# Kernel optimization log

Hardware: AMD Instinct MI355X
Metric: run time of the kernel (lower is better)

Reference implementation:

```python
import jax, jax.numpy as jnp
import numpy as np

N_NODES = 50000


def _gcn_layer(x, W, b, src, dst, n_nodes):
    # x: [N, Fin] -> h: [N, Fout]
    h = x @ W
    # symmetric normalization deg^{-1/2} A_hat deg^{-1/2} (self-loops already in src/dst)
    deg = jax.ops.segment_sum(jnp.ones(src.shape[0], h.dtype), dst, num_segments=n_nodes)
    dis = jnp.where(deg > 0, jax.lax.rsqrt(deg), jnp.zeros_like(deg))
    norm = dis[src] * dis[dst]  # [E]
    msg = h[src] * norm[:, None]  # [E, Fout]
    out = jax.ops.segment_sum(msg, dst, num_segments=n_nodes)
    return out + b


def setup_inputs() -> dict:
    key = jax.random.key(0)
    k1, k2, k3, k4 = jax.random.split(key, 4)
    in_ch, hid, out_ch = 128, 128, 64
    x = jax.random.normal(k1, (N_NODES, in_ch), dtype=jnp.float32)
    edge_index = jax.random.randint(k2, (2, 800000), 0, N_NODES, dtype=jnp.int64)
    # glorot-style init for the linear weights
    W1 = jax.random.normal(k3, (in_ch, hid), dtype=jnp.float32) * (1.0 / np.sqrt(in_ch))
    b1 = jnp.zeros((hid,), dtype=jnp.float32)
    W2 = jax.random.normal(k4, (hid, out_ch), dtype=jnp.float32) * (1.0 / np.sqrt(hid))
    b2 = jnp.zeros((out_ch,), dtype=jnp.float32)
    return {"x": x, "edge_index": edge_index, "W1": W1, "b1": b1, "W2": W2, "b2": b2}


def reference(x, edge_index, W1, b1, W2, b2):
    n = x.shape[0]
    loops = jnp.arange(n, dtype=edge_index.dtype)
    src = jnp.concatenate([edge_index[0], loops])
    dst = jnp.concatenate([edge_index[1], loops])
    h = jnp.tanh(_gcn_layer(x, W1, b1, src, dst, n))
    return _gcn_layer(h, W2, b2, src, dst, n)
```

## Files before the change

### kernel.cpp

```cpp
#include <hip/hip_runtime.h>
#include <hip/hip_fp16.h>
#include <math.h>


__global__ __launch_bounds__(256) void normalize_kernel(const int* __restrict__ ei32,
                                                        int* __restrict__ out, int n2,
                                                        int* __restrict__ hist, int nh) {
    __shared__ int s_is64;
    if (threadIdx.x == 0) {
        int is64 = 1;
        for (int k = 1; k < 64; k += 2)
            if (ei32[k] != 0) { is64 = 0; break; }
        s_is64 = is64;
    }
    __syncthreads();
    const int is64 = s_is64;
    for (int i = blockIdx.x * blockDim.x + threadIdx.x; i < n2;
         i += gridDim.x * blockDim.x) {
        out[i] = is64 ? ei32[2 * i] : ei32[i];
        if (i < nh) hist[i] = 0;
    }
}

__global__ __launch_bounds__(256) void hist_kernel(const int* __restrict__ dst, int E,
                                                   int* __restrict__ hist) {
    for (int i = blockIdx.x * blockDim.x + threadIdx.x; i < E;
         i += gridDim.x * blockDim.x) {
        atomicAdd(&hist[dst[i]], 1);
    }
}

__global__ __launch_bounds__(256) void scan1_kernel(const int* __restrict__ hist,
                                                    int* __restrict__ row_start,
                                                    int* __restrict__ partial, int n) {
    __shared__ int tmp[256];
    int t = threadIdx.x;
    int i = blockIdx.x * 256 + t;
    int v = (i < n) ? hist[i] : 0;
    tmp[t] = v;
    __syncthreads();
    for (int off = 1; off < 256; off <<= 1) {
        int add = (t >= off) ? tmp[t - off] : 0;
        __syncthreads();
        tmp[t] += add;
        __syncthreads();
    }
    if (i < n) row_start[i] = tmp[t] - v;
    if (t == 255) partial[blockIdx.x] = tmp[255];
}

__global__ __launch_bounds__(256) void scan23_kernel(int* __restrict__ row_start,
                                                     const int* __restrict__ partial,
                                                     const int* __restrict__ hist,
                                                     float* __restrict__ dis,
                                                     int* __restrict__ cursor,
                                                     int n, int E, int nb) {
    __shared__ int offs[256];
    int t = threadIdx.x;
    int v = (t < nb) ? partial[t] : 0;
    offs[t] = v;
    __syncthreads();
    for (int off = 1; off < 256; off <<= 1) {
        int add = (t >= off) ? offs[t - off] : 0;
        __syncthreads();
        offs[t] += add;
        __syncthreads();
    }
    int incl = offs[t];
    __syncthreads();
    offs[t] = incl - v;
    __syncthreads();

    int i = blockIdx.x * 256 + t;
    if (i < n) {
        row_start[i] += offs[i >> 8];
        dis[i] = rsqrtf((float)(hist[i] + 1));
        cursor[i] = 0;
    }
    if (i == 0) row_start[n] = E;
}

__global__ __launch_bounds__(256) void scatter_kernel(const int* __restrict__ src,
                                                      const int* __restrict__ dst, int E,
                                                      const int* __restrict__ row_start,
                                                      int* __restrict__ cursor,
                                                      int* __restrict__ csr_src) {
    for (int i = blockIdx.x * blockDim.x + threadIdx.x; i < E;
         i += gridDim.x * blockDim.x) {
        int d = dst[i];
        int pos = atomicAdd(&cursor[d], 1);
        csr_src[row_start[d] + pos] = src[i];
    }
}

template <int BM, int BN, int TM, int TN, bool HALF_OUT>
__global__ __launch_bounds__(256) void gemm_tile(const float* __restrict__ A,
                                                 const float* __restrict__ B,
                                                 const float* __restrict__ scale,
                                                 void* __restrict__ Cv,
                                                 int M, int K, int N) {
    constexpr int BK = 32;
    constexpr int TX = BN / TN;
    constexpr int TY = BM / TM;
    static_assert(TX * TY == 256, "256 threads");
    const int t = threadIdx.x;
    const int tx = t % TX;
    const int ty = t / TX;
    const int row0 = blockIdx.x * BM;

    __shared__ float As[BK][BM + 4];
    __shared__ float Bs[BK][BN + 4];

    float acc[TM][TN];
#pragma unroll
    for (int i = 0; i < TM; i++)
#pragma unroll
        for (int j = 0; j < TN; j++) acc[i][j] = 0.f;

    for (int k0 = 0; k0 < K; k0 += BK) {
        constexpr int A4 = BM * BK / 4;
#pragma unroll
        for (int idx4 = t; idx4 < A4; idx4 += 256) {
            int r = idx4 / (BK / 4);
            int c4 = idx4 % (BK / 4);
            float4 v = make_float4(0.f, 0.f, 0.f, 0.f);
            int gr = row0 + r;
            if (gr < M) v = *(const float4*)&A[(size_t)gr * K + k0 + c4 * 4];
            As[c4 * 4 + 0][r] = v.x;
            As[c4 * 4 + 1][r] = v.y;
            As[c4 * 4 + 2][r] = v.z;
            As[c4 * 4 + 3][r] = v.w;
        }
        constexpr int B4 = BK * BN / 4;
#pragma unroll
        for (int idx4 = t; idx4 < B4; idx4 += 256) {
            int r = idx4 / (BN / 4);
            int c4 = idx4 % (BN / 4);
            float4 v = *(const float4*)&B[(size_t)(k0 + r) * N + c4 * 4];
            *(float4*)&Bs[r][c4 * 4] = v;
        }
        __syncthreads();

#pragma unroll 4
        for (int kk = 0; kk < BK; kk++) {
            float a[TM], b[TN];
#pragma unroll
            for (int i = 0; i < TM; i += 4)
                *(float4*)&a[i] = *(const float4*)&As[kk][ty * TM + i];
#pragma unroll
            for (int j = 0; j < TN; j += 4)
                *(float4*)&b[j] = *(const float4*)&Bs[kk][tx * TN + j];
#pragma unroll
            for (int i = 0; i < TM; i++)
#pragma unroll
                for (int j = 0; j < TN; j++) acc[i][j] += a[i] * b[j];
        }
        __syncthreads();
    }

#pragma unroll
    for (int i = 0; i < TM; i++) {
        int gr = row0 + ty * TM + i;
        if (gr < M) {
            float sc = scale[gr];
            if constexpr (HALF_OUT) {
                __half* C = (__half*)Cv;
                __half2 tmp[TN / 2];
#pragma unroll
                for (int j = 0; j < TN; j += 2)
                    tmp[j / 2] = __floats2half2_rn(acc[i][j] * sc, acc[i][j + 1] * sc);
                if constexpr (TN == 8) {
                    *(float4*)&C[(size_t)gr * N + tx * TN] = *(float4*)tmp;
                } else {
                    *(float2*)&C[(size_t)gr * N + tx * TN] = *(float2*)tmp;
                }
            } else {
                float* C = (float*)Cv;
#pragma unroll
                for (int j = 0; j < TN; j += 4) {
                    float4 v = make_float4(acc[i][j] * sc, acc[i][j + 1] * sc,
                                           acc[i][j + 2] * sc, acc[i][j + 3] * sc);
                    *(float4*)&C[(size_t)gr * N + tx * TN + j] = v;
                }
            }
        }
    }
}

__global__ __launch_bounds__(256) void agg1_kernel(const __half* __restrict__ hs,
                                                   const float* __restrict__ dis,
                                                   const int* __restrict__ row_start,
                                                   const int* __restrict__ csr_src,
                                                   const float* __restrict__ b1,
                                                   float* __restrict__ hout, int n) {
    const int wid = threadIdx.x >> 6;
    const int lane = threadIdx.x & 63;
    const __half2* hv = (const __half2*)hs;

    for (int node = blockIdx.x * 4 + wid; node < n; node += gridDim.x * 4) {
        float2 acc = __half22float2(hv[(size_t)node * 64 + lane]);

        const int e0 = row_start[node];
        const int deg = row_start[node + 1] - e0;

        for (int base = 0; base < deg; base += 64) {
            const int cnt = min(64, deg - base);
            int myidx = 0;
            if (lane < cnt) myidx = csr_src[e0 + base + lane];

            int k = 0;
            for (; k + 8 <= cnt; k += 8) {
                int s0 = __shfl(myidx, k + 0);
                int s1 = __shfl(myidx, k + 1);
                int s2 = __shfl(myidx, k + 2);
                int s3 = __shfl(myidx, k + 3);
                int s4 = __shfl(myidx, k + 4);
                int s5 = __shfl(myidx, k + 5);
                int s6 = __shfl(myidx, k + 6);
                int s7 = __shfl(myidx, k + 7);
                float2 v0 = __half22float2(hv[(size_t)s0 * 64 + lane]);
                float2 v1 = __half22float2(hv[(size_t)s1 * 64 + lane]);
                float2 v2 = __half22float2(hv[(size_t)s2 * 64 + lane]);
                float2 v3 = __half22float2(hv[(size_t)s3 * 64 + lane]);
                float2 v4 = __half22float2(hv[(size_t)s4 * 64 + lane]);
                float2 v5 = __half22float2(hv[(size_t)s5 * 64 + lane]);
                float2 v6 = __half22float2(hv[(size_t)s6 * 64 + lane]);
                float2 v7 = __half22float2(hv[(size_t)s7 * 64 + lane]);
                acc.x += ((v0.x + v1.x) + (v2.x + v3.x)) + ((v4.x + v5.x) + (v6.x + v7.x));
                acc.y += ((v0.y + v1.y) + (v2.y + v3.y)) + ((v4.y + v5.y) + (v6.y + v7.y));
            }
            for (; k < cnt; ++k) {
                int s = __shfl(myidx, k);
                float2 v = __half22float2(hv[(size_t)s * 64 + lane]);
                acc.x += v.x;
                acc.y += v.y;
            }
        }
        float dd = dis[node];
        float2 bb = ((const float2*)b1)[lane];
        float2 o;
        o.x = tanhf(acc.x * dd + bb.x);
        o.y = tanhf(acc.y * dd + bb.y);
        ((float2*)hout)[(size_t)node * 64 + lane] = o;
    }
}

__global__ __launch_bounds__(256) void agg2_kernel(const __half* __restrict__ hs,
                                                   const float* __restrict__ dis,
                                                   const int* __restrict__ row_start,
                                                   const int* __restrict__ csr_src,
                                                   const float* __restrict__ b2,
                                                   float* __restrict__ out, int n) {
    const int wid = threadIdx.x >> 6;
    const int lane = threadIdx.x & 63;

    for (int node = blockIdx.x * 4 + wid; node < n; node += gridDim.x * 4) {
        float acc = __half2float(hs[(size_t)node * 64 + lane]);

        const int e0 = row_start[node];
        const int deg = row_start[node + 1] - e0;

        for (int base = 0; base < deg; base += 64) {
            const int cnt = min(64, deg - base);
            int myidx = 0;
            if (lane < cnt) myidx = csr_src[e0 + base + lane];

            int k = 0;
            for (; k + 8 <= cnt; k += 8) {
                int s0 = __shfl(myidx, k + 0);
                int s1 = __shfl(myidx, k + 1);
                int s2 = __shfl(myidx, k + 2);
                int s3 = __shfl(myidx, k + 3);
                int s4 = __shfl(myidx, k + 4);
                int s5 = __shfl(myidx, k + 5);
                int s6 = __shfl(myidx, k + 6);
                int s7 = __shfl(myidx, k + 7);
                float v0 = __half2float(hs[(size_t)s0 * 64 + lane]);
                float v1 = __half2float(hs[(size_t)s1 * 64 + lane]);
                float v2 = __half2float(hs[(size_t)s2 * 64 + lane]);
                float v3 = __half2float(hs[(size_t)s3 * 64 + lane]);
                float v4 = __half2float(hs[(size_t)s4 * 64 + lane]);
                float v5 = __half2float(hs[(size_t)s5 * 64 + lane]);
                float v6 = __half2float(hs[(size_t)s6 * 64 + lane]);
                float v7 = __half2float(hs[(size_t)s7 * 64 + lane]);
                acc += ((v0 + v1) + (v2 + v3)) + ((v4 + v5) + (v6 + v7));
            }
            for (; k < cnt; ++k) {
                int s = __shfl(myidx, k);
                acc += __half2float(hs[(size_t)s * 64 + lane]);
            }
        }
        out[(size_t)node * 64 + lane] = acc * dis[node] + b2[lane];
    }
}

extern "C" void kernel_launch(void* const* d_in, const int* in_sizes, int n_in,
                              void* d_out, int out_size, void* d_ws, size_t ws_size,
                              hipStream_t stream) {
    const float* x  = (const float*)d_in[0];
    const int*   ei = (const int*)d_in[1];
    const float* W1 = (const float*)d_in[2];
    const float* b1 = (const float*)d_in[3];
    const float* W2 = (const float*)d_in[4];
    const float* b2 = (const float*)d_in[5];

    const int hid    = in_sizes[3];
    const int in_ch  = in_sizes[2] / hid;
    const int out_ch = in_sizes[5];
    const int N      = in_sizes[0] / in_ch;
    const int E      = in_sizes[1] / 2;

    char* wsp = (char*)d_ws;
    auto alloc = [&](size_t bytes) -> char* {
        char* p = wsp;
        wsp += (bytes + 255) & ~(size_t)255;
        return p;
    };
    __half* h1       = (__half*)alloc((size_t)N * hid * 2);
    float*  hmid     = (float*)alloc((size_t)N * hid * 4);
    __half* h2       = (__half*)alloc((size_t)N * out_ch * 2);
    int*   hist      = (int*)alloc((size_t)N * 4);
    int*   cursor    = (int*)alloc((size_t)N * 4);
    int*   row_start = (int*)alloc((size_t)(N + 1) * 4);
    float* dis       = (float*)alloc((size_t)N * 4);
    int*   partial   = (int*)alloc(1024);
    int*   enorm     = (int*)alloc((size_t)2 * E * 4);
    int*   csr_src   = (int*)alloc((size_t)E * 4);

    const int NB = (N + 255) / 256;

    normalize_kernel<<<2048, 256, 0, stream>>>(ei, enorm, 2 * E, hist, N);
    const int* esrc = enorm;
    const int* edst = enorm + E;

    hist_kernel<<<1024, 256, 0, stream>>>(edst, E, hist);
    scan1_kernel<<<NB, 256, 0, stream>>>(hist, row_start, partial, N);
    scan23_kernel<<<NB, 256, 0, stream>>>(row_start, partial, hist, dis, cursor, N, E, NB);
    scatter_kernel<<<1024, 256, 0, stream>>>(esrc, edst, E, row_start, cursor, csr_src);

    gemm_tile<128, 128, 8, 8, true><<<(N + 127) / 128, 256, 0, stream>>>(
        x, W1, dis, h1, N, in_ch, hid);
    agg1_kernel<<<2048, 256, 0, stream>>>(h1, dis, row_start, csr_src, b1, hmid, N);

    gemm_tile<128, 64, 8, 4, true><<<(N + 127) / 128, 256, 0, stream>>>(
        hmid, W2, dis, h2, N, hid, out_ch);
    agg2_kernel<<<2048, 256, 0, stream>>>(h2, dis, row_start, csr_src, b2,
                                          (float*)d_out, N);
}
```

Before: 275.7 us.

## Use fp16 MFMA GEMMs and store the hidden layer in half precision

```diff
diff --git a/kernel.cpp b/kernel.cpp
--- a/kernel.cpp
+++ b/kernel.cpp
@@ -2,6 +2,9 @@
 #include <hip/hip_fp16.h>
 #include <math.h>
 
+
+typedef _Float16 fh8 __attribute__((ext_vector_type(8)));
+typedef float f4 __attribute__((ext_vector_type(4)));
 
 __global__ __launch_bounds__(256) void normalize_kernel(const int* __restrict__ ei32,
                                                         int* __restrict__ out, int n2,
@@ -93,95 +96,98 @@
     }
 }
 
-template <int BM, int BN, int TM, int TN, bool HALF_OUT>
-__global__ __launch_bounds__(256) void gemm_tile(const float* __restrict__ A,
-                                                 const float* __restrict__ B,
+__global__ __launch_bounds__(256) void prep_w_kernel(const float* __restrict__ W1,
+                                                     const float* __restrict__ W2,
+                                                     __half* __restrict__ w1t,
+                                                     __half* __restrict__ w2t,
+                                                     int K, int N1, int N2) {
+    int total1 = K * N1, total2 = K * N2;
+    for (int i = blockIdx.x * 256 + threadIdx.x; i < total1 + total2;
+         i += gridDim.x * 256) {
+        if (i < total1) {
+            int c = i / K, k = i % K;
+            w1t[i] = __float2half(W1[(size_t)k * N1 + c]);
+        } else {
+            int j = i - total1;
+            int c = j / K, k = j % K;
+            w2t[j] = __float2half(W2[(size_t)k * N2 + c]);
+        }
+    }
+}
+
+template <int BN, bool AH>
+__global__ __launch_bounds__(256) void gemm_mfma(const void* __restrict__ Av,
+                                                 const __half* __restrict__ WT,
                                                  const float* __restrict__ scale,
-                                                 void* __restrict__ Cv,
-                                                 int M, int K, int N) {
-    constexpr int BK = 32;
-    constexpr int TX = BN / TN;
-    constexpr int TY = BM / TM;
-    static_assert(TX * TY == 256, "256 threads");
+                                                 __half* __restrict__ C, int M) {
+    constexpr int K = 128;
+    constexpr int LDK = K + 8;
     const int t = threadIdx.x;
-    const int tx = t % TX;
-    const int ty = t / TX;
-    const int row0 = blockIdx.x * BM;
-
-    __shared__ float As[BK][BM + 4];
-    __shared__ float Bs[BK][BN + 4];
-
-    float acc[TM][TN];
-#pragma unroll
-    for (int i = 0; i < TM; i++)
-#pragma unroll
-        for (int j = 0; j < TN; j++) acc[i][j] = 0.f;
-
-    for (int k0 = 0; k0 < K; k0 += BK) {
-        constexpr int A4 = BM * BK / 4;
-#pragma unroll
-        for (int idx4 = t; idx4 < A4; idx4 += 256) {
-            int r = idx4 / (BK / 4);
-            int c4 = idx4 % (BK / 4);
-            float4 v = make_float4(0.f, 0.f, 0.f, 0.f);
-            int gr = row0 + r;
-            if (gr < M) v = *(const float4*)&A[(size_t)gr * K + k0 + c4 * 4];
-            As[c4 * 4 + 0][r] = v.x;
-            As[c4 * 4 + 1][r] = v.y;
-            As[c4 * 4 + 2][r] = v.z;
-            As[c4 * 4 + 3][r] = v.w;
-        }
-        constexpr int B4 = BK * BN / 4;
-#pragma unroll
-        for (int idx4 = t; idx4 < B4; idx4 += 256) {
-            int r = idx4 / (BN / 4);
-            int c4 = idx4 % (BN / 4);
-            float4 v = *(const float4*)&B[(size_t)(k0 + r) * N + c4 * 4];
-            *(float4*)&Bs[r][c4 * 4] = v;
-        }
-        __syncthreads();
-
-#pragma unroll 4
-        for (int kk = 0; kk < BK; kk++) {
-            float a[TM], b[TN];
-#pragma unroll
-            for (int i = 0; i < TM; i += 4)
-                *(float4*)&a[i] = *(const float4*)&As[kk][ty * TM + i];
-#pragma unroll
-            for (int j = 0; j < TN; j += 4)
-                *(float4*)&b[j] = *(const float4*)&Bs[kk][tx * TN + j];
-#pragma unroll
-            for (int i = 0; i < TM; i++)
-#pragma unroll
-                for (int j = 0; j < TN; j++) acc[i][j] += a[i] * b[j];
-        }
-        __syncthreads();
-    }
-
-#pragma unroll
-    for (int i = 0; i < TM; i++) {
-        int gr = row0 + ty * TM + i;
-        if (gr < M) {
-            float sc = scale[gr];
-            if constexpr (HALF_OUT) {
-                __half* C = (__half*)Cv;
-                __half2 tmp[TN / 2];
-#pragma unroll
-                for (int j = 0; j < TN; j += 2)
-                    tmp[j / 2] = __floats2half2_rn(acc[i][j] * sc, acc[i][j + 1] * sc);
-                if constexpr (TN == 8) {
-                    *(float4*)&C[(size_t)gr * N + tx * TN] = *(float4*)tmp;
-                } else {
-                    *(float2*)&C[(size_t)gr * N + tx * TN] = *(float2*)tmp;
-                }
+    const int wv = t >> 6;
+    const int lane = t & 63;
+    const int row0 = blockIdx.x * 64;
+
+    __shared__ __half As[4][16][LDK];
+    __shared__ __half Ws[BN][LDK];
+
+    {
+        constexpr int V = BN * K / 8;
+        for (int i = t; i < V; i += 256) {
+            int c = i / (K / 8);
+            int v8 = i % (K / 8);
+            fh8 w = *(const fh8*)&WT[(size_t)c * K + v8 * 8];
+            *(fh8*)&Ws[c][v8 * 8] = w;
+        }
+    }
+    {
+        for (int idx = lane; idx < 16 * 64; idx += 64) {
+            int r = idx >> 6;
+            int c2 = idx & 63;
+            int grow = row0 + wv * 16 + r;
+            __half2 h;
+            if (AH) {
+                h = (grow < M) ? ((const __half2*)Av)[(size_t)grow * 64 + c2]
+                               : __floats2half2_rn(0.f, 0.f);
             } else {
-                float* C = (float*)Cv;
-#pragma unroll
-                for (int j = 0; j < TN; j += 4) {
-                    float4 v = make_float4(acc[i][j] * sc, acc[i][j + 1] * sc,
-                                           acc[i][j + 2] * sc, acc[i][j + 3] * sc);
-                    *(float4*)&C[(size_t)gr * N + tx * TN + j] = v;
-                }
+                float2 f = make_float2(0.f, 0.f);
+                if (grow < M) f = ((const float2*)Av)[(size_t)grow * 64 + c2];
+                h = __floats2half2_rn(f.x, f.y);
+            }
+            *(__half2*)&As[wv][r][c2 * 2] = h;
+        }
+    }
+    __syncthreads();
+
+    const int lr = lane & 15;
+    const int lk = (lane >> 4) * 8;
+
+    fh8 af[4];
+#pragma unroll
+    for (int ks = 0; ks < 4; ks++)
+        af[ks] = *(const fh8*)&As[wv][lr][ks * 32 + lk];
+
+    f4 acc[BN / 16];
+#pragma unroll
+    for (int nt = 0; nt < BN / 16; nt++) acc[nt] = (f4){0.f, 0.f, 0.f, 0.f};
+
+#pragma unroll
+    for (int nt = 0; nt < BN / 16; nt++) {
+#pragma unroll
+        for (int ks = 0; ks < 4; ks++) {
+            fh8 bf = *(const fh8*)&Ws[nt * 16 + lr][ks * 32 + lk];
+            acc[nt] = __builtin_amdgcn_mfma_f32_16x16x32_f16(af[ks], bf, acc[nt], 0, 0, 0);
+        }
+    }
+
+    const int rbase = row0 + wv * 16 + (lane >> 4) * 4;
+#pragma unroll
+    for (int j = 0; j < 4; j++) {
+        int grow = rbase + j;
+        if (grow < M) {
+            float sc = scale[grow];
+#pragma unroll
+            for (int nt = 0; nt < BN / 16; nt++) {
+                C[(size_t)grow * BN + nt * 16 + lr] = __float2half(acc[nt][j] * sc);
             }
         }
     }
@@ -192,7 +198,7 @@
                                                    const int* __restrict__ row_start,
                                                    const int* __restrict__ csr_src,
                                                    const float* __restrict__ b1,
-                                                   float* __restrict__ hout, int n) {
+                                                   __half* __restrict__ hout, int n) {
     const int wid = threadIdx.x >> 6;
     const int lane = threadIdx.x & 63;
     const __half2* hv = (const __half2*)hs;
@@ -238,10 +244,8 @@
         }
         float dd = dis[node];
         float2 bb = ((const float2*)b1)[lane];
-        float2 o;
-        o.x = tanhf(acc.x * dd + bb.x);
-        o.y = tanhf(acc.y * dd + bb.y);
-        ((float2*)hout)[(size_t)node * 64 + lane] = o;
+        ((__half2*)hout)[(size_t)node * 64 + lane] =
+            __floats2half2_rn(tanhf(acc.x * dd + bb.x), tanhf(acc.y * dd + bb.y));
     }
 }
 
@@ -317,8 +321,10 @@
         return p;
     };
     __half* h1       = (__half*)alloc((size_t)N * hid * 2);
-    float*  hmid     = (float*)alloc((size_t)N * hid * 4);
+    __half* hmid     = (__half*)alloc((size_t)N * hid * 2);
     __half* h2       = (__half*)alloc((size_t)N * out_ch * 2);
+    __half* w1t      = (__half*)alloc((size_t)hid * in_ch * 2);
+    __half* w2t      = (__half*)alloc((size_t)out_ch * hid * 2);
     int*   hist      = (int*)alloc((size_t)N * 4);
     int*   cursor    = (int*)alloc((size_t)N * 4);
     int*   row_start = (int*)alloc((size_t)(N + 1) * 4);
@@ -330,6 +336,7 @@
     const int NB = (N + 255) / 256;
 
     normalize_kernel<<<2048, 256, 0, stream>>>(ei, enorm, 2 * E, hist, N);
+    prep_w_kernel<<<96, 256, 0, stream>>>(W1, W2, w1t, w2t, in_ch, hid, out_ch);
     const int* esrc = enorm;
     const int* edst = enorm + E;
 
@@ -338,12 +345,10 @@
     scan23_kernel<<<NB, 256, 0, stream>>>(row_start, partial, hist, dis, cursor, N, E, NB);
     scatter_kernel<<<1024, 256, 0, stream>>>(esrc, edst, E, row_start, cursor, csr_src);
 
-    gemm_tile<128, 128, 8, 8, true><<<(N + 127) / 128, 256, 0, stream>>>(
-        x, W1, dis, h1, N, in_ch, hid);
+    gemm_mfma<128, false><<<(N + 63) / 64, 256, 0, stream>>>(x, w1t, dis, h1, N);
     agg1_kernel<<<2048, 256, 0, stream>>>(h1, dis, row_start, csr_src, b1, hmid, N);
 
-    gemm_tile<128, 64, 8, 4, true><<<(N + 127) / 128, 256, 0, stream>>>(
-        hmid, W2, dis, h2, N, hid, out_ch);
+    gemm_mfma<64, true><<<(N + 63) / 64, 256, 0, stream>>>(hmid, w2t, dis, h2, N);
     agg2_kernel<<<2048, 256, 0, stream>>>(h2, dis, row_start, csr_src, b2,
                                           (float*)d_out, N);
 }
```

Result: faster. 258.0 us (-6.4%).
